# Kernel optimization log

Measured on AMD Instinct MI355X. Metric: run time of the kernel, lower is better.

Reference implementation:

```python
import jax, jax.numpy as jnp
import numpy as np

D_DIST = 1.5       # init kwarg d_dist
NUM_LABELS = 64    # K; labels drawn from [0, K), all present w.h.p. at N=200k
B, C, N = 8, 32, 200000


def setup_inputs() -> dict:
    key = jax.random.key(0)
    k1, k2 = jax.random.split(key)
    prediction = jax.random.normal(k1, (B, C, N), dtype=jnp.float32)
    label = jax.random.randint(k2, (B, N), 0, NUM_LABELS)
    return {"prediction": prediction, "label": label}


def _batch_loss(pred, lab):
    # pred: [C, N], lab: [N] int in [0, K)
    K = NUM_LABELS
    counts = jax.ops.segment_sum(jnp.ones(lab.shape, pred.dtype), lab, num_segments=K)  # [K]
    sums = jax.ops.segment_sum(pred.T, lab, num_segments=K)                              # [K, C]
    center = sums / jnp.maximum(counts, 1.0)[:, None]                                    # [K, C] per-label mean
    # square_distance_single(center, center): pairwise sq-dist between the C columns
    # of center (coordinates are the K cluster axes) -> [C, C], exactly as the torch code.
    gram = center.T @ center                       # [C, C]
    n2 = jnp.sum(center * center, axis=0)          # [C]
    sq = jax.nn.relu(n2[:, None] + n2[None, :] - 2.0 * gram)
    # safe sqrt: identical forward to sqrt(relu(sq)) but finite grads at 0
    dist = jnp.where(sq > 0, jnp.sqrt(jnp.where(sq > 0, sq, 1.0)), 0.0)
    hinge = jax.nn.relu(2.0 * D_DIST - dist)
    return jnp.sum(hinge * hinge) / (2.0 * K * (K - 1.0 + 1e-16))


def reference(prediction, label):
    # sum over batches, matching the python loop accumulation
    return jnp.sum(jax.vmap(_batch_loss)(prediction, label))
```

## Files before the change

kernel.cpp:

```cpp
#include <hip/hip_runtime.h>
#include <stdint.h>

#define BATCH    8
#define CDIM     32
#define KLBL     64
#define NPB      200000
#define SLABS_PB 6250
#define CHUNKS   96

typedef __attribute__((ext_vector_type(8))) short bf16x8;
typedef __attribute__((ext_vector_type(4))) float f32x4;

union ABits { uint32_t u[4]; bf16x8 v; };

__device__ __forceinline__ uint32_t cvtpk_bf16(float lo, float hi) {
  uint32_t r;
  asm volatile("v_cvt_pk_bf16_f32 %0, %1, %2" : "=v"(r) : "v"(lo), "v"(hi));
  return r;
}

__global__ __launch_bounds__(256) void seg_mfma_kernel(
    const float* __restrict__ pred,
    const int*   __restrict__ label,
    float* __restrict__ gsums,
    float* __restrict__ gcounts) {
  __shared__ float s_part[4][KLBL * CDIM + KLBL];

  const int tid = threadIdx.x;
  const int wv = tid >> 6;
  const int ln = tid & 63;
  const int chunk = blockIdx.x, b = blockIdx.y;

  const int s0 = (int)((long long)chunk * SLABS_PB / CHUNKS);
  const int s1 = (int)((long long)(chunk + 1) * SLABS_PB / CHUNKS);
  const int w0 = s0 + (int)((long long)(s1 - s0) * wv / 4);
  const int w1 = s0 + (int)((long long)(s1 - s0) * (wv + 1) / 4);

  const int crow = ln & 15;
  const int kseg = (ln >> 4) * 8;

  const float* row0 = pred + ((size_t)b * CDIM + crow) * NPB;
  const float* row1 = pred + ((size_t)b * CDIM + crow + 16) * NPB;
  const int*   labp = label + (size_t)b * NPB;

  ABits ones;
  ones.u[0] = ones.u[1] = ones.u[2] = ones.u[3] = 0x3F803F80u;

  f32x4 acc[4][2];
  f32x4 accc[4];
#pragma unroll
  for (int kt = 0; kt < 4; ++kt) {
    acc[kt][0] = (f32x4){0.f, 0.f, 0.f, 0.f};
    acc[kt][1] = (f32x4){0.f, 0.f, 0.f, 0.f};
    accc[kt]   = (f32x4){0.f, 0.f, 0.f, 0.f};
  }

  float4 fA0, fA1, fA2, fA3;  int4 lA0, lA1;
  float4 fB0, fB1, fB2, fB3;  int4 lB0, lB1;

  auto loadA = [&](int s) {
    const int n0 = s * 32 + kseg;
    fA0 = *(const float4*)(row0 + n0);
    fA1 = *(const float4*)(row0 + n0 + 4);
    fA2 = *(const float4*)(row1 + n0);
    fA3 = *(const float4*)(row1 + n0 + 4);
    lA0 = *(const int4*)(labp + n0);
    lA1 = *(const int4*)(labp + n0 + 4);
  };
  auto loadB = [&](int s) {
    const int n0 = s * 32 + kseg;
    fB0 = *(const float4*)(row0 + n0);
    fB1 = *(const float4*)(row0 + n0 + 4);
    fB2 = *(const float4*)(row1 + n0);
    fB3 = *(const float4*)(row1 + n0 + 4);
    lB0 = *(const int4*)(labp + n0);
    lB1 = *(const int4*)(labp + n0 + 4);
  };

  ABits b0v, b1v, av[4];

  auto derive = [&](const float4& f0, const float4& f1, const float4& f2,
                    const float4& f3, const int4& l0, const int4& l1) {
    b0v.u[0] = cvtpk_bf16(f0.x, f0.y);
    b0v.u[1] = cvtpk_bf16(f0.z, f0.w);
    b0v.u[2] = cvtpk_bf16(f1.x, f1.y);
    b0v.u[3] = cvtpk_bf16(f1.z, f1.w);
    b1v.u[0] = cvtpk_bf16(f2.x, f2.y);
    b1v.u[1] = cvtpk_bf16(f2.z, f2.w);
    b1v.u[2] = cvtpk_bf16(f3.x, f3.y);
    b1v.u[3] = cvtpk_bf16(f3.z, f3.w);
#pragma unroll
    for (int kt = 0; kt < 4; ++kt) {
      const int tgt = kt * 16 + crow;
      av[kt].u[0] = (l0.x == tgt ? 0x3F80u : 0u) | (l0.y == tgt ? 0x3F800000u : 0u);
      av[kt].u[1] = (l0.z == tgt ? 0x3F80u : 0u) | (l0.w == tgt ? 0x3F800000u : 0u);
      av[kt].u[2] = (l1.x == tgt ? 0x3F80u : 0u) | (l1.y == tgt ? 0x3F800000u : 0u);
      av[kt].u[3] = (l1.z == tgt ? 0x3F80u : 0u) | (l1.w == tgt ? 0x3F800000u : 0u);
    }
  };

  auto mfma_step = [&]() {
#pragma unroll
    for (int kt = 0; kt < 4; ++kt) {
      acc[kt][0] = __builtin_amdgcn_mfma_f32_16x16x32_bf16(av[kt].v, b0v.v, acc[kt][0], 0, 0, 0);
      acc[kt][1] = __builtin_amdgcn_mfma_f32_16x16x32_bf16(av[kt].v, b1v.v, acc[kt][1], 0, 0, 0);
      accc[kt]   = __builtin_amdgcn_mfma_f32_16x16x32_bf16(av[kt].v, ones.v, accc[kt], 0, 0, 0);
    }
  };

  if (w0 < w1) loadA(w0);
  if (w0 + 1 < w1) loadB(w0 + 1);

  int s = w0;
  while (s < w1) {
    derive(fA0, fA1, fA2, fA3, lA0, lA1);
    if (s + 2 < w1) loadA(s + 2);
    __builtin_amdgcn_sched_barrier(0);
    mfma_step();
    ++s;
    if (s >= w1) break;
    derive(fB0, fB1, fB2, fB3, lB0, lB1);
    if (s + 2 < w1) loadB(s + 2);
    __builtin_amdgcn_sched_barrier(0);
    mfma_step();
    ++s;
  }

#pragma unroll
  for (int kt = 0; kt < 4; ++kt) {
#pragma unroll
    for (int r = 0; r < 4; ++r) {
      const int k = kt * 16 + (ln >> 4) * 4 + r;
      s_part[wv][k * CDIM + crow]      = acc[kt][0][r];
      s_part[wv][k * CDIM + 16 + crow] = acc[kt][1][r];
      if (crow == 0) s_part[wv][KLBL * CDIM + k] = accc[kt][r];
    }
  }
  __syncthreads();

  float* gs = gsums + (size_t)b * KLBL * CDIM;
  for (int i = tid; i < KLBL * CDIM + KLBL; i += 256) {
    const float v = s_part[0][i] + s_part[1][i] + s_part[2][i] + s_part[3][i];
    if (i < KLBL * CDIM) atomicAdd(&gs[i], v);
    else                 atomicAdd(&gcounts[b * KLBL + (i - KLBL * CDIM)], v);
  }
}

__global__ __launch_bounds__(256) void loss_kernel(
    const float* __restrict__ gsums,
    const float* __restrict__ gcounts,
    float* __restrict__ out) {
  const int b = blockIdx.x;
  __shared__ float s_center[KLBL * CDIM];
  __shared__ float s_red[256];

  for (int i = threadIdx.x; i < KLBL * CDIM; i += 256) {
    const float cnt = fmaxf(gcounts[b * KLBL + (i >> 5)], 1.0f);
    s_center[i] = gsums[(size_t)b * KLBL * CDIM + i] / cnt;
  }
  __syncthreads();

  float acc = 0.f;
  for (int p = threadIdx.x; p < CDIM * CDIM; p += 256) {
    const int i = p >> 5, j = p & 31;
    float g = 0.f, ni = 0.f, nj = 0.f;
#pragma unroll
    for (int k = 0; k < KLBL; ++k) {
      const float ci = s_center[k * CDIM + i];
      const float cj = s_center[k * CDIM + j];
      g += ci * cj;
      ni += ci * ci;
      nj += cj * cj;
    }
    float sq = fmaxf(ni + nj - 2.f * g, 0.f);
    const float dist = (sq > 0.f) ? sqrtf(sq) : 0.f;
    const float h = fmaxf(3.0f - dist, 0.f);
    acc += h * h;
  }

  s_red[threadIdx.x] = acc;
  __syncthreads();
  for (int s = 128; s > 0; s >>= 1) {
    if (threadIdx.x < s) s_red[threadIdx.x] += s_red[threadIdx.x + s];
    __syncthreads();
  }
  if (threadIdx.x == 0)
    atomicAdd(out, s_red[0] / (2.0f * (float)KLBL * ((float)KLBL - 1.0f)));
}

extern "C" void kernel_launch(void* const* d_in, const int* in_sizes, int n_in,
                              void* d_out, int out_size, void* d_ws, size_t ws_size,
                              hipStream_t stream) {
  const float* pred  = (const float*)d_in[0];
  const int*   label = (const int*)d_in[1];
  float* out = (float*)d_out;

  float* gsums   = (float*)d_ws;
  float* gcounts = gsums + (size_t)BATCH * KLBL * CDIM;

  const size_t accum_bytes =
      (size_t)(BATCH * KLBL * CDIM + BATCH * KLBL) * sizeof(float);
  hipMemsetAsync(d_ws, 0, accum_bytes, stream);
  hipMemsetAsync(d_out, 0, sizeof(float), stream);

  dim3 grid1(CHUNKS, BATCH);
  seg_mfma_kernel<<<grid1, 256, 0, stream>>>(pred, label, gsums, gcounts);

  loss_kernel<<<BATCH, 256, 0, stream>>>(gsums, gcounts, out);
}
```

Baseline: 65.39 us.

## Replace global atomics and memsets with per-chunk partials reduced in loss kernel

Each segment block now writes its per-chunk sums and counts to a private slot in the workspace instead of issuing atomicAdds, and the loss kernel reduces the 64 chunk partials per batch before computing centers. The two hipMemsetAsync calls are removed, and the first block zeroes the output instead. The chunk count drops from 96 to 64 to shrink the partial buffer. The loss kernel, which runs only 8 blocks, now reads about 64x more data serially, which adds latency to the tail stage.

```diff
diff --git a/kernel.cpp b/kernel.cpp
--- a/kernel.cpp
+++ b/kernel.cpp
@@ -1,12 +1,13 @@
 #include <hip/hip_runtime.h>
 #include <stdint.h>
 
-#define BATCH    8
-#define CDIM     32
-#define KLBL     64
-#define NPB      200000
-#define SLABS_PB 6250
-#define CHUNKS   96
+#define BATCH   8
+#define CDIM    32
+#define KLBL    64
+#define NPB     200000
+#define SLABS   6250
+#define CHUNKS  64
+#define REC     (KLBL * CDIM + KLBL)
 
 typedef __attribute__((ext_vector_type(8))) short bf16x8;
 typedef __attribute__((ext_vector_type(4))) float f32x4;
@@ -22,17 +23,19 @@
 __global__ __launch_bounds__(256) void seg_mfma_kernel(
     const float* __restrict__ pred,
     const int*   __restrict__ label,
-    float* __restrict__ gsums,
-    float* __restrict__ gcounts) {
-  __shared__ float s_part[4][KLBL * CDIM + KLBL];
+    float* __restrict__ partial,
+    float* __restrict__ out) {
+  __shared__ float s_part[4][REC];
 
   const int tid = threadIdx.x;
   const int wv = tid >> 6;
   const int ln = tid & 63;
   const int chunk = blockIdx.x, b = blockIdx.y;
 
-  const int s0 = (int)((long long)chunk * SLABS_PB / CHUNKS);
-  const int s1 = (int)((long long)(chunk + 1) * SLABS_PB / CHUNKS);
+  if (chunk == 0 && b == 0 && tid == 0) out[0] = 0.f;
+
+  const int s0 = (int)((long long)chunk * SLABS / CHUNKS);
+  const int s1 = (int)((long long)(chunk + 1) * SLABS / CHUNKS);
   const int w0 = s0 + (int)((long long)(s1 - s0) * wv / 4);
   const int w1 = s0 + (int)((long long)(s1 - s0) * (wv + 1) / 4);
 
@@ -138,41 +141,44 @@
   }
   __syncthreads();
 
-  float* gs = gsums + (size_t)b * KLBL * CDIM;
-  for (int i = tid; i < KLBL * CDIM + KLBL; i += 256) {
-    const float v = s_part[0][i] + s_part[1][i] + s_part[2][i] + s_part[3][i];
-    if (i < KLBL * CDIM) atomicAdd(&gs[i], v);
-    else                 atomicAdd(&gcounts[b * KLBL + (i - KLBL * CDIM)], v);
-  }
+  float* dst = partial + ((size_t)b * CHUNKS + chunk) * REC;
+  for (int i = tid; i < REC; i += 256)
+    dst[i] = s_part[0][i] + s_part[1][i] + s_part[2][i] + s_part[3][i];
 }
 
 __global__ __launch_bounds__(256) void loss_kernel(
-    const float* __restrict__ gsums,
-    const float* __restrict__ gcounts,
+    const float* __restrict__ partial,
     float* __restrict__ out) {
   const int b = blockIdx.x;
-  __shared__ float s_center[KLBL * CDIM];
+  __shared__ float s_rec[REC];
   __shared__ float s_red[256];
 
+  const float* src = partial + (size_t)b * CHUNKS * REC;
+  for (int i = threadIdx.x; i < REC; i += 256) {
+    float s = 0.f;
+    for (int ch = 0; ch < CHUNKS; ++ch) s += src[(size_t)ch * REC + i];
+    s_rec[i] = s;
+  }
+  __syncthreads();
   for (int i = threadIdx.x; i < KLBL * CDIM; i += 256) {
-    const float cnt = fmaxf(gcounts[b * KLBL + (i >> 5)], 1.0f);
-    s_center[i] = gsums[(size_t)b * KLBL * CDIM + i] / cnt;
+    const float cnt = fmaxf(s_rec[KLBL * CDIM + (i >> 5)], 1.0f);
+    s_rec[i] = s_rec[i] / cnt;
   }
   __syncthreads();
 
   float acc = 0.f;
   for (int p = threadIdx.x; p < CDIM * CDIM; p += 256) {
     const int i = p >> 5, j = p & 31;
-    float g = 0.f, ni = 0.f, nj = 0.f;
+    float gr = 0.f, ni = 0.f, nj = 0.f;
 #pragma unroll
     for (int k = 0; k < KLBL; ++k) {
-      const float ci = s_center[k * CDIM + i];
-      const float cj = s_center[k * CDIM + j];
-      g += ci * cj;
+      const float ci = s_rec[k * CDIM + i];
+      const float cj = s_rec[k * CDIM + j];
+      gr += ci * cj;
       ni += ci * ci;
       nj += cj * cj;
     }
-    float sq = fmaxf(ni + nj - 2.f * g, 0.f);
+    float sq = fmaxf(ni + nj - 2.f * gr, 0.f);
     const float dist = (sq > 0.f) ? sqrtf(sq) : 0.f;
     const float h = fmaxf(3.0f - dist, 0.f);
     acc += h * h;
@@ -195,16 +201,9 @@
   const int*   label = (const int*)d_in[1];
   float* out = (float*)d_out;
 
-  float* gsums   = (float*)d_ws;
-  float* gcounts = gsums + (size_t)BATCH * KLBL * CDIM;
-
-  const size_t accum_bytes =
-      (size_t)(BATCH * KLBL * CDIM + BATCH * KLBL) * sizeof(float);
-  hipMemsetAsync(d_ws, 0, accum_bytes, stream);
-  hipMemsetAsync(d_out, 0, sizeof(float), stream);
+  float* partial = (float*)d_ws;
 
   dim3 grid1(CHUNKS, BATCH);
-  seg_mfma_kernel<<<grid1, 256, 0, stream>>>(pred, label, gsums, gcounts);
-
-  loss_kernel<<<BATCH, 256, 0, stream>>>(gsums, gcounts, out);
-}
+  seg_mfma_kernel<<<grid1, 256, 0, stream>>>(pred, label, partial, out);
+  loss_kernel<<<BATCH, 256, 0, stream>>>(partial, out);
+}
```

Result: slower. 70.76 us (+8.2%).
